# Optimization experiments

Hardware: AMD Instinct MI355X
Metric: run time of the kernel (lower is better)

## Reference

```python
import jax, jax.numpy as jnp
import numpy as np

B, S, D = 2, 2048, 1024
H = 16
HD = D // H  # 64, per-head size
EPS = 1e-5


def _ln(x, g, b):
    mu = jnp.mean(x, axis=-1, keepdims=True)
    var = jnp.var(x, axis=-1, keepdims=True)
    return (x - mu) * jax.lax.rsqrt(var + EPS) * g + b


def setup_inputs() -> dict:
    key = jax.random.key(0)
    ks = jax.random.split(key, 8)
    sd = 1.0 / np.sqrt(D)
    return {
        "x": jax.random.normal(ks[0], (B, S, D), jnp.float32),
        "w_qkv": jax.random.normal(ks[1], (3 * D, D), jnp.float32) * sd,
        "w_proj": jax.random.normal(ks[2], (D, D), jnp.float32) * sd,
        "b_proj": jnp.zeros((D,), jnp.float32),
        "w1": jax.random.normal(ks[3], (4 * D, D), jnp.float32) * sd,
        "b1": jnp.zeros((4 * D,), jnp.float32),
        "w2": jax.random.normal(ks[4], (D, 4 * D), jnp.float32) * (1.0 / np.sqrt(4 * D)),
        "b2": jnp.zeros((D,), jnp.float32),
        "ln1_g": jnp.ones((D,), jnp.float32),
        "ln1_b": jnp.zeros((D,), jnp.float32),
        "ln2_g": jnp.ones((D,), jnp.float32),
        "ln2_b": jnp.zeros((D,), jnp.float32),
    }


def reference(x, w_qkv, w_proj, b_proj, w1, b1, w2, b2, ln1_g, ln1_b, ln2_g, ln2_b):
    # --- pre-LN self-attention ---
    h = _ln(x, ln1_g, ln1_b)
    qkv = jnp.einsum("bsd,ed->bse", h, w_qkv)  # [B,S,3D]
    q, k, v = jnp.split(qkv, 3, axis=-1)
    # [B,H,S,HD]
    q = q.reshape(B, S, H, HD).transpose(0, 2, 1, 3)
    k = k.reshape(B, S, H, HD).transpose(0, 2, 1, 3)
    v = v.reshape(B, S, H, HD).transpose(0, 2, 1, 3)
    logits = jnp.einsum("bhqd,bhkd->bhqk", q, k) / np.sqrt(HD)
    probs = jax.nn.softmax(logits, axis=-1)  # no causal mask in non-flash path
    out = jnp.einsum("bhqk,bhkd->bhqd", probs, v)
    out = out.transpose(0, 2, 1, 3).reshape(B, S, D)
    out = jnp.einsum("bsd,ed->bse", out, w_proj) + b_proj
    x = x + out
    # --- pre-LN MLP ---
    h2 = _ln(x, ln2_g, ln2_b)
    h2 = jax.nn.relu(jnp.einsum("bsd,fd->bsf", h2, w1) + b1)
    h2 = jnp.einsum("bsf,df->bsd", h2, w2) + b2
    return x + h2
```

## Files before the change

kernel.cpp:

```cpp
#include <hip/hip_runtime.h>
#include <stdint.h>

typedef unsigned short ushort_t;
typedef __attribute__((ext_vector_type(8))) short s16x8;
typedef __attribute__((ext_vector_type(4))) float f32x4;

static __device__ __forceinline__ float bf2f(ushort_t u) {
  union { unsigned int i; float f; } x; x.i = ((unsigned int)u) << 16; return x.f;
}
static __device__ __forceinline__ ushort_t f2bf(float f) {
  union { float f; unsigned int i; } x; x.f = f;
  unsigned int r = (x.i + 0x7FFFu + ((x.i >> 16) & 1u)) >> 16;
  return (ushort_t)r;
}
static __device__ __forceinline__ unsigned f2bf_pos_u(float f) {
  return (__float_as_uint(f) + 0x8000u) >> 16;
}
static __device__ __forceinline__ bool nonfin(float f) {
  return (__float_as_uint(f) & 0x7F800000u) == 0x7F800000u;
}

static __device__ __forceinline__ float dpp_add16(float x) {
  float y;
  y = __int_as_float(__builtin_amdgcn_update_dpp(0, __float_as_int(x), 0xB1, 0xF, 0xF, true)); x += y;
  y = __int_as_float(__builtin_amdgcn_update_dpp(0, __float_as_int(x), 0x4E, 0xF, 0xF, true)); x += y;
  y = __int_as_float(__builtin_amdgcn_update_dpp(0, __float_as_int(x), 0x141, 0xF, 0xF, true)); x += y;
  y = __int_as_float(__builtin_amdgcn_update_dpp(0, __float_as_int(x), 0x140, 0xF, 0xF, true)); x += y;
  return x;
}

#define GLL16(gp, lp) __builtin_amdgcn_global_load_lds( \
    (const __attribute__((address_space(1))) void*)(gp), \
    (__attribute__((address_space(3))) void*)(lp), 16, 0, 0)

__global__ void zero_flags(int* flags) { if (threadIdx.x < 16) flags[threadIdx.x] = 0; }

__global__ void apply_flags(const int* __restrict__ flags, float* __restrict__ out) {
  int i = threadIdx.x;
  if (i < 7 && flags[i]) out[i] = 1.0e5f * (i + 1);
}

__global__ __launch_bounds__(256) void cvt2(
    const float* __restrict__ a, ushort_t* __restrict__ oa, int na_units,
    const float* __restrict__ b, ushort_t* __restrict__ ob) {
  int u = blockIdx.x * 256 + threadIdx.x;
  const float* in; ushort_t* out; size_t off;
  if (u < na_units) { in = a; out = oa; off = (size_t)u * 8; }
  else              { in = b; out = ob; off = (size_t)(u - na_units) * 8; }
  f32x4 x0 = *(const f32x4*)(in + off);
  f32x4 x1 = *(const f32x4*)(in + off + 4);
  s16x8 o;
#pragma unroll
  for (int j = 0; j < 4; j++) { o[j] = f2bf(x0[j]); o[4 + j] = f2bf(x1[j]); }
  *(s16x8*)(out + off) = o;
}

__global__ __launch_bounds__(256) void ln_kernel(
    const float* __restrict__ x, const float* __restrict__ g,
    const float* __restrict__ b, ushort_t* __restrict__ o,
    int* __restrict__ flags, int flag_idx) {
  int row = blockIdx.x;
  int tid = threadIdx.x;
  const float* xr = x + (size_t)row * 1024;
  f32x4 v = *(const f32x4*)(xr + tid * 4);
  float s = 0.f, ss = 0.f;
#pragma unroll
  for (int j = 0; j < 4; j++) { s += v[j]; ss += v[j] * v[j]; }
#pragma unroll
  for (int off = 32; off > 0; off >>= 1) {
    s += __shfl_xor(s, off);
    ss += __shfl_xor(ss, off);
  }
  __shared__ float red[8];
  int wave = tid >> 6, lane = tid & 63;
  if (lane == 0) { red[wave] = s; red[4 + wave] = ss; }
  __syncthreads();
  s = red[0] + red[1] + red[2] + red[3];
  ss = red[4] + red[5] + red[6] + red[7];
  float mu = s * (1.f / 1024.f);
  float var = ss * (1.f / 1024.f) - mu * mu;
  float rstd = rsqrtf(var + 1e-5f);
  f32x4 gg = *(const f32x4*)(g + tid * 4);
  f32x4 bb = *(const f32x4*)(b + tid * 4);
  ushort_t* orow = o + (size_t)row * 1024 + tid * 4;
#pragma unroll
  for (int j = 0; j < 4; j++) {
    float vv = (v[j] - mu) * rstd * gg[j] + bb[j];
    if (nonfin(vv)) { atomicOr(flags + flag_idx, 1); vv = 0.f; }
    orow[j] = f2bf(vv);
  }
}

template <int BM, int EPI>
__global__ __launch_bounds__(256) void gemm_bt(
    const ushort_t* __restrict__ A, const ushort_t* __restrict__ Bt,
    const float* __restrict__ bias, const float* __restrict__ res,
    ushort_t* __restrict__ Cb, float* __restrict__ Cf,
    int M, int N, int K, int lda, int ldb) {
  constexpr int AM = BM / 32;
  constexpr int ACH = (BM * 64) / (256 * 8);
  __shared__ ushort_t sA[BM * 64];
  __shared__ ushort_t sB[128 * 64];
  int tid = threadIdx.x;
  int wave = tid >> 6, lane = tid & 63;
  int wm = wave >> 1, wn = wave & 1;
  int bm = blockIdx.x, bn = blockIdx.y;
  int g = lane >> 4, r = lane & 15;
  int rx8 = (r & 7) << 3;

  const ushort_t* gA[ACH];
  ushort_t* lA[ACH];
#pragma unroll
  for (int c = 0; c < ACH; c++) {
    int e = wave * (BM * 16) + c * 512 + lane * 8;
    int row = e >> 6, col = e & 63;
    gA[c] = A + (size_t)(bm * BM + row) * lda + (col ^ ((row & 7) << 3));
    lA[c] = sA + wave * (BM * 16) + c * 512;
  }
  const ushort_t* gB[4];
  ushort_t* lB[4];
#pragma unroll
  for (int c = 0; c < 4; c++) {
    int e = wave * 2048 + c * 512 + lane * 8;
    int row = e >> 6, col = e & 63;
    gB[c] = Bt + (size_t)(bn * 128 + row) * ldb + (col ^ ((row & 7) << 3));
    lB[c] = sB + wave * 2048 + c * 512;
  }

  f32x4 acc[AM][4];
#pragma unroll
  for (int m = 0; m < AM; m++)
#pragma unroll
    for (int n = 0; n < 4; n++) acc[m][n] = (f32x4){0.f, 0.f, 0.f, 0.f};

  for (int k0 = 0; k0 < K; k0 += 64) {
#pragma unroll
    for (int c = 0; c < ACH; c++) { GLL16(gA[c], lA[c]); gA[c] += 64; }
#pragma unroll
    for (int c = 0; c < 4; c++) { GLL16(gB[c], lB[c]); gB[c] += 64; }
    __syncthreads();
#pragma unroll
    for (int kk = 0; kk < 2; kk++) {
      int cx = (kk * 32 + g * 8) ^ rx8;
      s16x8 af[AM], bfr[4];
#pragma unroll
      for (int m = 0; m < AM; m++)
        af[m] = *(const s16x8*)&sA[(wm * (BM / 2) + m * 16 + r) * 64 + cx];
#pragma unroll
      for (int n = 0; n < 4; n++)
        bfr[n] = *(const s16x8*)&sB[(wn * 64 + n * 16 + r) * 64 + cx];
#pragma unroll
      for (int m = 0; m < AM; m++)
#pragma unroll
        for (int n = 0; n < 4; n++)
          acc[m][n] = __builtin_amdgcn_mfma_f32_16x16x32_bf16(af[m], bfr[n], acc[m][n], 0, 0, 0);
    }
    __syncthreads();
  }

#pragma unroll
  for (int n = 0; n < 4; n++) {
    int colg = bn * 128 + wn * 64 + n * 16 + r;
    float bv = (EPI == 2 || EPI == 6) ? bias[colg] : 0.f;
#pragma unroll
    for (int m = 0; m < AM; m++) {
#pragma unroll
      for (int q = 0; q < 4; q++) {
        int rowg = bm * BM + wm * (BM / 2) + m * 16 + g * 4 + q;
        size_t idx = (size_t)rowg * N + colg;
        float vv = acc[m][n][q] + bv;
        if (EPI == 2) vv = fmaxf(vv, 0.f);
        if (EPI == 6) vv += res[idx];
        if (EPI == 9) vv += Cf[idx];
        if (EPI == 6 || EPI == 9) Cf[idx] = vv;
        else Cb[idx] = f2bf(vv);
      }
    }
  }
}

__global__ __launch_bounds__(256) void attn_kernel(
    const ushort_t* __restrict__ qkv, ushort_t* __restrict__ out,
    int* __restrict__ flags) {
  __shared__ ushort_t sK[2][64 * 72];
  __shared__ ushort_t sVt[2][64 * 72];
  __shared__ ushort_t sP[128 * 72];
  int tid = threadIdx.x, wave = tid >> 6, lane = tid & 63;
  int g = lane >> 4, r = lane & 15;
  int bh = blockIdx.x, qt = blockIdx.y;
  int b = bh >> 4, h = bh & 15;
  const ushort_t* base = qkv + (size_t)b * 2048 * 3072 + h * 64;
  const ushort_t* qb = base;
  const ushort_t* kb = base + 1024;
  const ushort_t* vb = base + 2048;
  int q0 = qt * 128;
  const float SC = 0.125f * 1.44269504f;

  int srow = tid >> 3;
  int scol = (tid & 7) * 8;

  s16x8 aq[2][2];
#pragma unroll
  for (int t = 0; t < 2; t++)
#pragma unroll
    for (int hh = 0; hh < 2; hh++)
      aq[t][hh] = *(const s16x8*)(qb + (size_t)(q0 + wave * 32 + t * 16 + r) * 3072 + hh * 32 + g * 8);

  f32x4 O[2][4];
  float l_r[2][4];
#pragma unroll
  for (int t = 0; t < 2; t++)
#pragma unroll
    for (int n = 0; n < 4; n++) O[t][n] = (f32x4){0.f, 0.f, 0.f, 0.f};
#pragma unroll
  for (int t = 0; t < 2; t++)
#pragma unroll
    for (int qq = 0; qq < 4; qq++) l_r[t][qq] = 0.f;

  {
    const ushort_t* kr = kb + (size_t)srow * 3072 + scol;
    s16x8 k0 = *(const s16x8*)kr;
    s16x8 k1 = *(const s16x8*)(kr + (size_t)32 * 3072);
    const ushort_t* vp = vb + (size_t)srow * 3072 + scol;
    s16x8 v0 = *(const s16x8*)vp;
    s16x8 v1 = *(const s16x8*)(vp + (size_t)32 * 3072);
    *(s16x8*)&sK[0][srow * 72 + scol] = k0;
    *(s16x8*)&sK[0][(srow + 32) * 72 + scol] = k1;
#pragma unroll
    for (int j = 0; j < 8; j++) {
      unsigned w = ((unsigned)(unsigned short)v0[j]) | (((unsigned)(unsigned short)v1[j]) << 16);
      *(unsigned*)&sVt[0][(scol + j) * 72 + srow * 2] = w;
    }
  }

  for (int kt = 0; kt < 32; ++kt) {
    int cur = kt & 1;
    __syncthreads();

    s16x8 nk0 = {}, nk1 = {}, nv0 = {}, nv1 = {};
    if (kt < 31) {
      int kv0n = (kt + 1) * 64;
      const ushort_t* kr = kb + (size_t)(kv0n + srow) * 3072 + scol;
      nk0 = *(const s16x8*)kr;
      nk1 = *(const s16x8*)(kr + (size_t)32 * 3072);
      const ushort_t* vp = vb + (size_t)(kv0n + srow) * 3072 + scol;
      nv0 = *(const s16x8*)vp;
      nv1 = *(const s16x8*)(vp + (size_t)32 * 3072);
    }

    f32x4 sc[2][4];
    __builtin_amdgcn_s_setprio(1);
#pragma unroll
    for (int n = 0; n < 4; n++) {
      s16x8 bk0 = *(const s16x8*)&sK[cur][(n * 16 + r) * 72 + g * 8];
      s16x8 bk1 = *(const s16x8*)&sK[cur][(n * 16 + r) * 72 + 32 + g * 8];
#pragma unroll
      for (int t = 0; t < 2; t++) {
        f32x4 z = (f32x4){0.f, 0.f, 0.f, 0.f};
        z = __builtin_amdgcn_mfma_f32_16x16x32_bf16(aq[t][0], bk0, z, 0, 0, 0);
        z = __builtin_amdgcn_mfma_f32_16x16x32_bf16(aq[t][1], bk1, z, 0, 0, 0);
        sc[t][n] = z;
      }
    }
    __builtin_amdgcn_s_setprio(0);

    if (kt < 31) {
      *(s16x8*)&sK[cur ^ 1][srow * 72 + scol] = nk0;
      *(s16x8*)&sK[cur ^ 1][(srow + 32) * 72 + scol] = nk1;
#pragma unroll
      for (int j = 0; j < 8; j++) {
        unsigned w = ((unsigned)(unsigned short)nv0[j]) | (((unsigned)(unsigned short)nv1[j]) << 16);
        *(unsigned*)&sVt[cur ^ 1][(scol + j) * 72 + srow * 2] = w;
      }
    }

#pragma unroll
    for (int t = 0; t < 2; t++) {
#pragma unroll
      for (int qq = 0; qq < 4; qq++) {
        float p0 = exp2f(sc[t][0][qq] * SC);
        float p1 = exp2f(sc[t][1][qq] * SC);
        float p2 = exp2f(sc[t][2][qq] * SC);
        float p3 = exp2f(sc[t][3][qq] * SC);
        l_r[t][qq] += (p0 + p1) + (p2 + p3);
        int qr = wave * 32 + t * 16 + g * 4 + qq;
        *(unsigned*)&sP[qr * 72 + 2 * r]      = f2bf_pos_u(p0) | (f2bf_pos_u(p2) << 16);
        *(unsigned*)&sP[qr * 72 + 32 + 2 * r] = f2bf_pos_u(p1) | (f2bf_pos_u(p3) << 16);
      }
    }

    s16x8 pa[2][2];
#pragma unroll
    for (int t = 0; t < 2; t++) {
      int qr2 = wave * 32 + t * 16 + r;
      pa[t][0] = *(const s16x8*)&sP[qr2 * 72 + g * 8];
      pa[t][1] = *(const s16x8*)&sP[qr2 * 72 + 32 + g * 8];
    }
    __builtin_amdgcn_s_setprio(1);
#pragma unroll
    for (int n = 0; n < 4; n++) {
      int dd = n * 16 + r;
      s16x8 bv0 = *(const s16x8*)&sVt[cur][dd * 72 + g * 8];
      s16x8 bv1 = *(const s16x8*)&sVt[cur][dd * 72 + 32 + g * 8];
#pragma unroll
      for (int t = 0; t < 2; t++) {
        O[t][n] = __builtin_amdgcn_mfma_f32_16x16x32_bf16(pa[t][0], bv0, O[t][n], 0, 0, 0);
        O[t][n] = __builtin_amdgcn_mfma_f32_16x16x32_bf16(pa[t][1], bv1, O[t][n], 0, 0, 0);
      }
    }
    __builtin_amdgcn_s_setprio(0);
  }

#pragma unroll
  for (int t = 0; t < 2; t++) {
#pragma unroll
    for (int qq = 0; qq < 4; qq++) {
      float li = 1.f / dpp_add16(l_r[t][qq]);
#pragma unroll
      for (int n = 0; n < 4; n++) {
        float vv = O[t][n][qq] * li;
        if (nonfin(vv)) { atomicOr(flags + 3, 1); vv = 0.f; }
        int rowg = b * 2048 + q0 + wave * 32 + t * 16 + g * 4 + qq;
        int colg = h * 64 + n * 16 + r;
        out[(size_t)rowg * 1024 + colg] = f2bf(vv);
      }
    }
  }
}

extern "C" void kernel_launch(void* const* d_in, const int* in_sizes, int n_in,
                              void* d_out, int out_size, void* d_ws, size_t ws_size,
                              hipStream_t stream) {
  const float* x      = (const float*)d_in[0];
  const float* w_qkv  = (const float*)d_in[1];
  const float* w_proj = (const float*)d_in[2];
  const float* b_proj = (const float*)d_in[3];
  const float* w1     = (const float*)d_in[4];
  const float* b1     = (const float*)d_in[5];
  const float* w2     = (const float*)d_in[6];
  const float* b2     = (const float*)d_in[7];
  const float* ln1g   = (const float*)d_in[8];
  const float* ln1b   = (const float*)d_in[9];
  const float* ln2g   = (const float*)d_in[10];
  const float* ln2b   = (const float*)d_in[11];
  float* outp = (float*)d_out;
  char* wsb = (char*)d_ws;

  const size_t MB = 1024 * 1024;
  int*      flags  = (int*)wsb;
  ushort_t* wqkvb  = (ushort_t*)(wsb + 1 * MB);
  ushort_t* wprojb = (ushort_t*)(wsb + 7 * MB);
  ushort_t* h1     = (ushort_t*)(wsb + 9 * MB);
  ushort_t* qkv    = (ushort_t*)(wsb + 17 * MB);
  ushort_t* attnb  = (ushort_t*)(wsb + 41 * MB);
  ushort_t* h2     = (ushort_t*)(wsb + 1 * MB);
  ushort_t* w1b    = (ushort_t*)(wsb + 9 * MB);
  ushort_t* w2b    = (ushort_t*)(wsb + 17 * MB);
  ushort_t* hmid   = (ushort_t*)(wsb + 25 * MB);
  bool single_mlp = (ws_size >= 57 * MB);

  dim3 blk(256);
  zero_flags<<<dim3(1), dim3(64), 0, stream>>>(flags);

  cvt2<<<dim3(2048), blk, 0, stream>>>(w_qkv, wqkvb, 393216, w_proj, wprojb);
  ln_kernel<<<dim3(4096), blk, 0, stream>>>(x, ln1g, ln1b, h1, flags, 0);
  gemm_bt<128, 0><<<dim3(32, 24), blk, 0, stream>>>(h1, wqkvb, nullptr, nullptr, qkv, nullptr,
                                                    4096, 3072, 1024, 1024, 1024);
  attn_kernel<<<dim3(32, 16), blk, 0, stream>>>(qkv, attnb, flags);

  cvt2<<<dim3(4096), blk, 0, stream>>>(w1, w1b, 524288, w2, w2b);

  gemm_bt<64, 6><<<dim3(64, 8), blk, 0, stream>>>(attnb, wprojb, b_proj, x, nullptr, outp,
                                                  4096, 1024, 1024, 1024, 1024);

  ln_kernel<<<dim3(4096), blk, 0, stream>>>(outp, ln2g, ln2b, h2, flags, 1);
  if (single_mlp) {
    gemm_bt<128, 2><<<dim3(32, 32), blk, 0, stream>>>(h2, w1b, b1, nullptr, hmid, nullptr,
                                                      4096, 4096, 1024, 1024, 1024);
    gemm_bt<64, 6><<<dim3(64, 8), blk, 0, stream>>>(hmid, w2b, b2, outp, nullptr, outp,
                                                    4096, 1024, 4096, 4096, 4096);
  } else {
    for (int fc = 0; fc < 2; ++fc) {
      gemm_bt<128, 2><<<dim3(32, 16), blk, 0, stream>>>(
          h2, w1b + (size_t)fc * 2048 * 1024, b1 + fc * 2048, nullptr, hmid, nullptr,
          4096, 2048, 1024, 1024, 1024);
      if (fc == 0)
        gemm_bt<64, 6><<<dim3(64, 8), blk, 0, stream>>>(
            hmid, w2b + fc * 2048, b2, outp, nullptr, outp,
            4096, 1024, 2048, 2048, 4096);
      else
        gemm_bt<64, 9><<<dim3(64, 8), blk, 0, stream>>>(
            hmid, w2b + fc * 2048, nullptr, nullptr, nullptr, outp,
            4096, 1024, 2048, 2048, 4096);
    }
  }
  apply_flags<<<dim3(1), dim3(64), 0, stream>>>(flags, outp);
}
```

Baseline: 266.9 us.

## Double-buffer GEMM LDS tiles with K-step 32 to overlap loads and MFMA

Switches the bf16 GEMM main loop from a single 64-wide K tile to two 32-wide LDS buffers, so the next tile is fetched while MFMAs run on the current one. The per-iteration barrier count drops from two to one, and the XOR swizzle changes to fit 32-column rows. In exchange, each iteration does half the MFMA work, so barrier overhead is spread over less compute, and the new swizzle may change LDS bank-conflict behaviour.

```diff
diff --git a/kernel.cpp b/kernel.cpp
--- a/kernel.cpp
+++ b/kernel.cpp
@@ -98,33 +98,34 @@
     ushort_t* __restrict__ Cb, float* __restrict__ Cf,
     int M, int N, int K, int lda, int ldb) {
   constexpr int AM = BM / 32;
-  constexpr int ACH = (BM * 64) / (256 * 8);
-  __shared__ ushort_t sA[BM * 64];
-  __shared__ ushort_t sB[128 * 64];
+  constexpr int ACH = (BM * 32) / (256 * 8);
+  __shared__ ushort_t sA[2][BM * 32];
+  __shared__ ushort_t sB[2][128 * 32];
   int tid = threadIdx.x;
   int wave = tid >> 6, lane = tid & 63;
   int wm = wave >> 1, wn = wave & 1;
   int bm = blockIdx.x, bn = blockIdx.y;
   int g = lane >> 4, r = lane & 15;
-  int rx8 = (r & 7) << 3;
+  int cx = (g * 8) ^ ((r & 3) << 3);
 
   const ushort_t* gA[ACH];
-  ushort_t* lA[ACH];
+  int lAoff[ACH];
 #pragma unroll
   for (int c = 0; c < ACH; c++) {
-    int e = wave * (BM * 16) + c * 512 + lane * 8;
-    int row = e >> 6, col = e & 63;
-    gA[c] = A + (size_t)(bm * BM + row) * lda + (col ^ ((row & 7) << 3));
-    lA[c] = sA + wave * (BM * 16) + c * 512;
-  }
-  const ushort_t* gB[4];
-  ushort_t* lB[4];
-#pragma unroll
-  for (int c = 0; c < 4; c++) {
-    int e = wave * 2048 + c * 512 + lane * 8;
-    int row = e >> 6, col = e & 63;
-    gB[c] = Bt + (size_t)(bn * 128 + row) * ldb + (col ^ ((row & 7) << 3));
-    lB[c] = sB + wave * 2048 + c * 512;
+    int e = (BM == 128) ? (wave * 1024 + c * 512 + lane * 8)
+                        : (wave * 512 + lane * 8);
+    int row = e >> 5, col = e & 31;
+    gA[c] = A + (size_t)(bm * BM + row) * lda + (col ^ ((row & 3) << 3));
+    lAoff[c] = (BM == 128) ? (wave * 1024 + c * 512) : (wave * 512);
+  }
+  const ushort_t* gB[2];
+  int lBoff[2];
+#pragma unroll
+  for (int c = 0; c < 2; c++) {
+    int e = wave * 1024 + c * 512 + lane * 8;
+    int row = e >> 5, col = e & 31;
+    gB[c] = Bt + (size_t)(bn * 128 + row) * ldb + (col ^ ((row & 3) << 3));
+    lBoff[c] = wave * 1024 + c * 512;
   }
 
   f32x4 acc[AM][4];
@@ -133,29 +134,34 @@
 #pragma unroll
     for (int n = 0; n < 4; n++) acc[m][n] = (f32x4){0.f, 0.f, 0.f, 0.f};
 
-  for (int k0 = 0; k0 < K; k0 += 64) {
-#pragma unroll
-    for (int c = 0; c < ACH; c++) { GLL16(gA[c], lA[c]); gA[c] += 64; }
-#pragma unroll
-    for (int c = 0; c < 4; c++) { GLL16(gB[c], lB[c]); gB[c] += 64; }
+#pragma unroll
+  for (int c = 0; c < ACH; c++) { GLL16(gA[c], sA[0] + lAoff[c]); gA[c] += 32; }
+#pragma unroll
+  for (int c = 0; c < 2; c++) { GLL16(gB[c], sB[0] + lBoff[c]); gB[c] += 32; }
+  __syncthreads();
+
+  int cur = 0;
+  for (int k0 = 0; k0 < K; k0 += 32) {
+    if (k0 + 32 < K) {
+#pragma unroll
+      for (int c = 0; c < ACH; c++) { GLL16(gA[c], sA[cur ^ 1] + lAoff[c]); gA[c] += 32; }
+#pragma unroll
+      for (int c = 0; c < 2; c++) { GLL16(gB[c], sB[cur ^ 1] + lBoff[c]); gB[c] += 32; }
+    }
+    s16x8 af[AM], bfr[4];
+#pragma unroll
+    for (int m = 0; m < AM; m++)
+      af[m] = *(const s16x8*)&sA[cur][(wm * (BM / 2) + m * 16 + r) * 32 + cx];
+#pragma unroll
+    for (int n = 0; n < 4; n++)
+      bfr[n] = *(const s16x8*)&sB[cur][(wn * 64 + n * 16 + r) * 32 + cx];
+#pragma unroll
+    for (int m = 0; m < AM; m++)
+#pragma unroll
+      for (int n = 0; n < 4; n++)
+        acc[m][n] = __builtin_amdgcn_mfma_f32_16x16x32_bf16(af[m], bfr[n], acc[m][n], 0, 0, 0);
     __syncthreads();
-#pragma unroll
-    for (int kk = 0; kk < 2; kk++) {
-      int cx = (kk * 32 + g * 8) ^ rx8;
-      s16x8 af[AM], bfr[4];
-#pragma unroll
-      for (int m = 0; m < AM; m++)
-        af[m] = *(const s16x8*)&sA[(wm * (BM / 2) + m * 16 + r) * 64 + cx];
-#pragma unroll
-      for (int n = 0; n < 4; n++)
-        bfr[n] = *(const s16x8*)&sB[(wn * 64 + n * 16 + r) * 64 + cx];
-#pragma unroll
-      for (int m = 0; m < AM; m++)
-#pragma unroll
-        for (int n = 0; n < 4; n++)
-          acc[m][n] = __builtin_amdgcn_mfma_f32_16x16x32_bf16(af[m], bfr[n], acc[m][n], 0, 0, 0);
-    }
-    __syncthreads();
+    cur ^= 1;
   }
 
 #pragma unroll
```

New measurement: 285.4 us. +6.9%, slower.
